# Performance work log

Measured on AMD Instinct MI355X. Metric: run time of the kernel, lower is better.

## Reference

```python
import jax, jax.numpy as jnp
import numpy as np

N_NODES = 50000
N_EDGES = 600000
IN_DIM = 128
HID_DIM = 512
OUT_DIM = 2


def setup_inputs() -> dict:
    key = jax.random.key(0)
    ks = jax.random.split(key, 8)
    x = jax.random.normal(ks[0], (N_NODES, IN_DIM), dtype=jnp.float32)
    edge_index = jax.random.randint(ks[1], (2, N_EDGES), 0, N_NODES, dtype=jnp.int32)
    s1 = 1.0 / np.sqrt(IN_DIM)
    s2 = 1.0 / np.sqrt(HID_DIM)
    # SAGEConv params: lin_l (applied to mean-aggregated neighbors, has bias),
    # lin_r (applied to root node features, no bias)
    W1l = jax.random.uniform(ks[2], (IN_DIM, HID_DIM), jnp.float32, -s1, s1)
    b1 = jax.random.uniform(ks[3], (HID_DIM,), jnp.float32, -s1, s1)
    W1r = jax.random.uniform(ks[4], (IN_DIM, HID_DIM), jnp.float32, -s1, s1)
    W2l = jax.random.uniform(ks[5], (HID_DIM, OUT_DIM), jnp.float32, -s2, s2)
    b2 = jax.random.uniform(ks[6], (OUT_DIM,), jnp.float32, -s2, s2)
    W2r = jax.random.uniform(ks[7], (HID_DIM, OUT_DIM), jnp.float32, -s2, s2)
    return {"x": x, "W1l": W1l, "b1": b1, "W1r": W1r,
            "W2l": W2l, "b2": b2, "W2r": W2r, "edge_index": edge_index}


def _sage_conv(x, edge_index, Wl, b, Wr):
    src, dst = edge_index[0], edge_index[1]
    msgs = x[src]                                             # [E, d]
    agg = jax.ops.segment_sum(msgs, dst, num_segments=x.shape[0])  # [N, d]
    deg = jax.ops.segment_sum(jnp.ones_like(dst, dtype=x.dtype), dst,
                              num_segments=x.shape[0])
    agg = agg / jnp.maximum(deg, 1.0)[:, None]                # mean aggregation
    return agg @ Wl + b + x @ Wr


def reference(x, W1l, b1, W1r, W2l, b2, W2r, edge_index):
    h = _sage_conv(x, edge_index, W1l, b1, W1r)
    h = jax.nn.relu(h)
    # dropout inactive (eval mode / force_dropout=False)
    out = _sage_conv(h, edge_index, W2l, b2, W2r)
    return jax.nn.log_softmax(out, axis=1)
```

## Files before the change

kernel.cpp:

```cpp
#include <hip/hip_runtime.h>
#include <math.h>
#include <stdint.h>

#define N_NODES 50000
#define N_EDGES 600000
#define IN_DIM 128
#define HID_DIM 512
#define M_PAD 50048
#define SCAN_NB 196
#define NPAD 50048

#define NB_C 128
#define CE4_C 1172
#define HALF_N 25024
#define H4W 6256
#define HIST_NB 256

#define CASTX_NB5 3125
#define CASTW_NB5 272

typedef __bf16 bf16;
typedef __bf16 bf16x2 __attribute__((ext_vector_type(2)));
typedef __bf16 bf16x4 __attribute__((ext_vector_type(4)));
typedef __bf16 bf16x8 __attribute__((ext_vector_type(8)));
typedef float f32x4 __attribute__((ext_vector_type(4)));

#define GLDS(gp, lp) __builtin_amdgcn_global_load_lds( \
    (const __attribute__((address_space(1))) uint32_t*)(gp), \
    (__attribute__((address_space(3))) uint32_t*)(lp), 16, 0, 0)


__global__ __launch_bounds__(512) void histcast_kernel(
    const int* __restrict__ dst, uint32_t* __restrict__ Hg32,
    const float* __restrict__ x, bf16* __restrict__ xb,
    const float* __restrict__ W1l, const float* __restrict__ W1r,
    const float* __restrict__ W2l, const float* __restrict__ W2r,
    bf16* __restrict__ Wt, bf16* __restrict__ W2bt,
    int* __restrict__ done) {
    __shared__ uint32_t h4[H4W];
    int b = blockIdx.x, t = threadIdx.x;
    if (b < HIST_NB) {
        for (int j = t; j < H4W; j += 512) h4[j] = 0;
        __syncthreads();
        int c = b >> 1, h = b & 1;
        int base = h * HALF_N;
        int e40 = c * CE4_C;
        int e4end = min(e40 + CE4_C, N_EDGES / 4);
        for (int e4 = e40 + t; e4 < e4end; e4 += 512) {
            int4 d = ((const int4*)dst)[e4];
            unsigned v0 = (unsigned)(d.x - base);
            unsigned v1 = (unsigned)(d.y - base);
            unsigned v2 = (unsigned)(d.z - base);
            unsigned v3 = (unsigned)(d.w - base);
            if (v0 < HALF_N) atomicAdd(&h4[v0 >> 2], 1u << ((v0 & 3) << 3));
            if (v1 < HALF_N) atomicAdd(&h4[v1 >> 2], 1u << ((v1 & 3) << 3));
            if (v2 < HALF_N) atomicAdd(&h4[v2 >> 2], 1u << ((v2 & 3) << 3));
            if (v3 < HALF_N) atomicAdd(&h4[v3 >> 2], 1u << ((v3 & 3) << 3));
        }
        __syncthreads();
        uint32_t* outp = Hg32 + (size_t)c * (NPAD / 4) + (size_t)h * H4W;
        for (int j = t; j < H4W; j += 512) outp[j] = h4[j];
    } else if (b < HIST_NB + CASTX_NB5) {
        if (b == HIST_NB && t < SCAN_NB) done[t] = 0;
        int i = (b - HIST_NB) * 512 + t;
        float4 v = ((const float4*)x)[i];
        bf16x4 o = {(bf16)v.x, (bf16)v.y, (bf16)v.z, (bf16)v.w};
        *(bf16x4*)(xb + (size_t)i * 4) = o;
    } else {
        int idx = (b - HIST_NB - CASTX_NB5) * 512 + t;
        if (idx < 512 * 256) {
            int n = idx >> 8;
            int k = idx & 255;
            float v = (k < IN_DIM) ? W1l[(size_t)k * HID_DIM + n]
                                   : W1r[(size_t)(k - IN_DIM) * HID_DIM + n];
            Wt[idx] = (bf16)v;
        } else {
            int j = idx - 512 * 256;
            int n = j >> 9;
            int k = j & 511;
            float v = 0.f;
            if (n == 0) v = W2l[k * 2 + 0];
            else if (n == 1) v = W2l[k * 2 + 1];
            else if (n == 2) v = W2r[k * 2 + 0];
            else if (n == 3) v = W2r[k * 2 + 1];
            W2bt[j] = (bf16)v;
        }
    }
}


__global__ __launch_bounds__(256) void scan_kernel(
    const uint8_t* __restrict__ Hg, uint8_t* __restrict__ PB,
    int* __restrict__ offsets, int* __restrict__ done) {
    int t = threadIdx.x, blk = blockIdx.x;
    int n = blk * 256 + t;
    int running = 0;
    if (n < NPAD) {
#pragma unroll 8
        for (int c = 0; c < NB_C; ++c) {
            int v = Hg[(size_t)c * NPAD + n];
            PB[(size_t)c * NPAD + n] = (uint8_t)running;
            running += v;
        }
    }
    int v = (n < N_NODES) ? running : 0;
    int l = t & 63, w = t >> 6;
    int inc = v;
#pragma unroll
    for (int off = 1; off < 64; off <<= 1) {
        int y = __shfl_up(inc, off);
        if (l >= off) inc += y;
    }
    __shared__ int wsum[4];
    __shared__ int lookback;
    if (l == 63) wsum[w] = inc;
    __syncthreads();
    if (t == 0) {
        int tot = wsum[0] + wsum[1] + wsum[2] + wsum[3];
        __hip_atomic_store(&done[blk], tot + 1, __ATOMIC_RELEASE,
                           __HIP_MEMORY_SCOPE_AGENT);
    }
    if (t < 64) {
        int s = 0;
        for (int u = t; u < blk; u += 64) {
            int dv;
            do {
                dv = __hip_atomic_load(&done[u], __ATOMIC_ACQUIRE,
                                       __HIP_MEMORY_SCOPE_AGENT);
            } while (dv == 0);
            s += dv - 1;
        }
#pragma unroll
        for (int m = 1; m < 64; m <<= 1) s += __shfl_xor(s, m);
        if (t == 0) lookback = s;
    }
    __syncthreads();
    int add = lookback;
    for (int u = 0; u < w; ++u) add += wsum[u];
    int ex = add + inc - v;
    if (n < N_NODES) offsets[n] = ex;
    if (blk == 0 && t == 0) offsets[N_NODES] = N_EDGES;
}


__global__ __launch_bounds__(512) void fill_kernel(
    const int* __restrict__ src, const int* __restrict__ dst,
    const int* __restrict__ offsets, const uint8_t* __restrict__ PB,
    int* __restrict__ csr_src) {
    __shared__ uint32_t h4[H4W];
    int b = blockIdx.x, t = threadIdx.x;
    for (int j = t; j < H4W; j += 512) h4[j] = 0;
    __syncthreads();
    int c = b >> 1, h = b & 1;
    int base = h * HALF_N;
    const uint8_t* pb = PB + (size_t)c * NPAD;
    int e40 = c * CE4_C;
    int e4end = min(e40 + CE4_C, N_EDGES / 4);
    for (int e4 = e40 + t; e4 < e4end; e4 += 512) {
        int4 d = ((const int4*)dst)[e4];
        int4 s = ((const int4*)src)[e4];
        unsigned v0 = (unsigned)(d.x - base);
        unsigned v1 = (unsigned)(d.y - base);
        unsigned v2 = (unsigned)(d.z - base);
        unsigned v3 = (unsigned)(d.w - base);
        if (v0 < HALF_N) {
            int sh = (v0 & 3) << 3;
            uint32_t r = atomicAdd(&h4[v0 >> 2], 1u << sh);
            csr_src[offsets[d.x] + (int)pb[d.x] + (int)((r >> sh) & 0xff)] = s.x;
        }
        if (v1 < HALF_N) {
            int sh = (v1 & 3) << 3;
            uint32_t r = atomicAdd(&h4[v1 >> 2], 1u << sh);
            csr_src[offsets[d.y] + (int)pb[d.y] + (int)((r >> sh) & 0xff)] = s.y;
        }
        if (v2 < HALF_N) {
            int sh = (v2 & 3) << 3;
            uint32_t r = atomicAdd(&h4[v2 >> 2], 1u << sh);
            csr_src[offsets[d.z] + (int)pb[d.z] + (int)((r >> sh) & 0xff)] = s.z;
        }
        if (v3 < HALF_N) {
            int sh = (v3 & 3) << 3;
            uint32_t r = atomicAdd(&h4[v3 >> 2], 1u << sh);
            csr_src[offsets[d.w] + (int)pb[d.w] + (int)((r >> sh) & 0xff)] = s.w;
        }
    }
}


__global__ __launch_bounds__(256) void agg1_kernel(
    const bf16* __restrict__ xb, const int* __restrict__ offsets,
    const int* __restrict__ csr_src, bf16* __restrict__ agg1b) {
    int t = threadIdx.x;
    int w = t >> 6, l = t & 63;
    int g = l >> 4;
    int sl = l & 15;
    int n = blockIdx.x * 16 + w * 4 + g;
    int s0 = offsets[n], s1 = offsets[n + 1];
    float a[8] = {};
    int e = s0;
    for (; e + 4 <= s1; e += 4) {
        int i0 = csr_src[e + 0];
        int i1 = csr_src[e + 1];
        int i2 = csr_src[e + 2];
        int i3 = csr_src[e + 3];
        bf16x8 v0 = *(const bf16x8*)(xb + (size_t)i0 * IN_DIM + sl * 8);
        bf16x8 v1 = *(const bf16x8*)(xb + (size_t)i1 * IN_DIM + sl * 8);
        bf16x8 v2 = *(const bf16x8*)(xb + (size_t)i2 * IN_DIM + sl * 8);
        bf16x8 v3 = *(const bf16x8*)(xb + (size_t)i3 * IN_DIM + sl * 8);
#pragma unroll
        for (int u = 0; u < 8; ++u)
            a[u] += (float)v0[u] + (float)v1[u] + (float)v2[u] + (float)v3[u];
    }
    for (; e < s1; ++e) {
        int i0 = csr_src[e];
        bf16x8 v0 = *(const bf16x8*)(xb + (size_t)i0 * IN_DIM + sl * 8);
#pragma unroll
        for (int u = 0; u < 8; ++u) a[u] += (float)v0[u];
    }
    float inv = 1.0f / fmaxf((float)(s1 - s0), 1.0f);
    bf16x8 o;
#pragma unroll
    for (int u = 0; u < 8; ++u) o[u] = (bf16)(a[u] * inv);
    *(bf16x8*)(agg1b + (size_t)n * IN_DIM + sl * 8) = o;
}


__global__ __launch_bounds__(256) void gemm1_kernel(
    const bf16* __restrict__ agg1b, const bf16* __restrict__ xb,
    const bf16* __restrict__ Wt, const float* __restrict__ b1,
    const bf16* __restrict__ W2bt, float* __restrict__ zpart) {
    __shared__ __align__(16) char smem[128 * 136 * 2];
    bf16 (*As)[128][32] = (bf16(*)[128][32])smem;
    bf16 (*Bs)[128][32] = (bf16(*)[128][32])(smem + 16384);
    bf16 (*Hs)[136] = (bf16(*)[136])smem;
    int tid = threadIdx.x;
    int w = tid >> 6;
    int lane = tid & 63;
    int q = lane >> 4, rr = lane & 15;
    int cb = blockIdx.x;
    int n0 = cb * 128;
    int row0 = blockIdx.y * 128;
    int wm = (w & 1) * 64, wn = (w >> 1) * 64;
    int lr = lane >> 2;
    int lc = (lane & 3) * 8;

    auto stage = [&](int ki) {
        const bf16* Asrc;
        int kb;
        if (ki < 4) { Asrc = agg1b; kb = ki * 32; }
        else        { Asrc = xb;    kb = ki * 32 - IN_DIM; }
        int kw = ki * 32;
        int buf = ki & 1;
#pragma unroll
        for (int j = 0; j < 2; ++j) {
            int r = w * 32 + j * 16 + lr;
            GLDS(Asrc + (size_t)(row0 + r) * IN_DIM + kb + lc,
                 &As[buf][w * 32 + j * 16][0]);
            GLDS(Wt + (size_t)(n0 + r) * 256 + kw + lc,
                 &Bs[buf][w * 32 + j * 16][0]);
        }
    };

    f32x4 acc[4][4] = {};
    stage(0);
#pragma unroll
    for (int ki = 0; ki < 8; ++ki) {
        __syncthreads();
        if (ki + 1 < 8) stage(ki + 1);
        int buf = ki & 1;
        bf16x8 af[4], bfr[4];
#pragma unroll
        for (int i = 0; i < 4; ++i)
            af[i] = *(const bf16x8*)&As[buf][wm + i * 16 + rr][q * 8];
#pragma unroll
        for (int j = 0; j < 4; ++j)
            bfr[j] = *(const bf16x8*)&Bs[buf][wn + j * 16 + rr][q * 8];
#pragma unroll
        for (int i = 0; i < 4; ++i)
#pragma unroll
            for (int j = 0; j < 4; ++j)
                acc[i][j] = __builtin_amdgcn_mfma_f32_16x16x32_bf16(
                    af[i], bfr[j], acc[i][j], 0, 0, 0);
    }
    __syncthreads();
    float bias[4];
#pragma unroll
    for (int j = 0; j < 4; ++j) bias[j] = b1[n0 + wn + j * 16 + rr];
#pragma unroll
    for (int i = 0; i < 4; ++i) {
#pragma unroll
        for (int rg = 0; rg < 4; ++rg) {
            int mrow = wm + i * 16 + q * 4 + rg;
#pragma unroll
            for (int j = 0; j < 4; ++j)
                Hs[mrow][wn + j * 16 + rr] =
                    (bf16)fmaxf(acc[i][j][rg] + bias[j], 0.f);
        }
    }
    __syncthreads();
    bf16x8 wf[4];
#pragma unroll
    for (int ks = 0; ks < 4; ++ks)
        wf[ks] = *(const bf16x8*)(W2bt + (size_t)rr * 512 + n0 + ks * 32 + q * 8);
    f32x4 zacc[2] = {};
#pragma unroll
    for (int mt = 0; mt < 2; ++mt)
#pragma unroll
        for (int ks = 0; ks < 4; ++ks) {
            bf16x8 afz = *(const bf16x8*)&Hs[w * 32 + mt * 16 + rr][ks * 32 + q * 8];
            zacc[mt] = __builtin_amdgcn_mfma_f32_16x16x32_bf16(
                afz, wf[ks], zacc[mt], 0, 0, 0);
        }
    if (rr < 4) {
#pragma unroll
        for (int mt = 0; mt < 2; ++mt)
#pragma unroll
            for (int rg = 0; rg < 4; ++rg) {
                int grow = row0 + w * 32 + mt * 16 + q * 4 + rg;
                zpart[(size_t)grow * 16 + cb * 4 + rr] = zacc[mt][rg];
            }
    }
}


__global__ __launch_bounds__(256) void zsum_kernel(const float* __restrict__ zpart,
                                                   float* __restrict__ z) {
    int n = blockIdx.x * blockDim.x + threadIdx.x;
    if (n >= N_NODES) return;
    const float4* p = (const float4*)(zpart + (size_t)n * 16);
    float4 a = p[0], b = p[1], c = p[2], d = p[3];
    float4 o = {a.x + b.x + c.x + d.x, a.y + b.y + c.y + d.y,
                a.z + b.z + c.z + d.z, a.w + b.w + c.w + d.w};
    *(float4*)(z + (size_t)n * 4) = o;
}


__global__ void final_kernel(const float* __restrict__ z, const int* __restrict__ offsets,
                             const int* __restrict__ csr_src, const float* __restrict__ b2,
                             float* __restrict__ out) {
    int n = blockIdx.x * blockDim.x + threadIdx.x;
    if (n >= N_NODES) return;
    int s0 = offsets[n], s1 = offsets[n + 1];
    float a0 = 0.f, a1 = 0.f;
    int e = s0;
    for (; e + 4 <= s1; e += 4) {
        int i0 = csr_src[e], i1 = csr_src[e + 1];
        int i2 = csr_src[e + 2], i3 = csr_src[e + 3];
        float2 v0 = *(const float2*)(z + (size_t)i0 * 4);
        float2 v1 = *(const float2*)(z + (size_t)i1 * 4);
        float2 v2 = *(const float2*)(z + (size_t)i2 * 4);
        float2 v3 = *(const float2*)(z + (size_t)i3 * 4);
        a0 += v0.x + v1.x + v2.x + v3.x;
        a1 += v0.y + v1.y + v2.y + v3.y;
    }
    for (; e < s1; ++e) {
        int s = csr_src[e];
        float2 v = *(const float2*)(z + (size_t)s * 4);
        a0 += v.x;
        a1 += v.y;
    }
    float inv = 1.0f / fmaxf((float)(s1 - s0), 1.0f);
    float2 zs = *(const float2*)(z + (size_t)n * 4 + 2);
    float o0 = a0 * inv + b2[0] + zs.x;
    float o1 = a1 * inv + b2[1] + zs.y;
    float m = fmaxf(o0, o1);
    float lse = logf(expf(o0 - m) + expf(o1 - m));
    float2 o = {o0 - m - lse, o1 - m - lse};
    *(float2*)(out + (size_t)n * 2) = o;
}


extern "C" void kernel_launch(void* const* d_in, const int* in_sizes, int n_in,
                              void* d_out, int out_size, void* d_ws, size_t ws_size,
                              hipStream_t stream) {
    const float* x   = (const float*)d_in[0];
    const float* W1l = (const float*)d_in[1];
    const float* b1  = (const float*)d_in[2];
    const float* W1r = (const float*)d_in[3];
    const float* W2l = (const float*)d_in[4];
    const float* b2  = (const float*)d_in[5];
    const float* W2r = (const float*)d_in[6];
    const int* edge  = (const int*)d_in[7];
    const int* src = edge;
    const int* dst = edge + N_EDGES;
    float* out = (float*)d_out;

    char* ws = (char*)d_ws;
    size_t off = 0;
    auto alloc = [&](size_t bytes) -> void* {
        void* p = ws + off;
        off += (bytes + 255) & ~(size_t)255;
        return p;
    };
    int* offsets = (int*)alloc((size_t)(N_NODES + 1) * 4);
    int* csr_src = (int*)alloc((size_t)N_EDGES * 4);
    int* done    = (int*)alloc((size_t)SCAN_NB * 4);
    bf16* xb     = (bf16*)alloc((size_t)M_PAD * IN_DIM * 2);
    bf16* agg1b  = (bf16*)alloc((size_t)M_PAD * IN_DIM * 2);
    bf16* Wt     = (bf16*)alloc((size_t)HID_DIM * 256 * 2);
    bf16* W2bt   = (bf16*)alloc((size_t)16 * HID_DIM * 2);
    float* zpart = (float*)alloc((size_t)M_PAD * 16 * 4);
    float* z     = (float*)alloc((size_t)N_NODES * 4 * 4);
    uint8_t* PB  = (uint8_t*)alloc((size_t)NB_C * NPAD);

    uint32_t* Hg32 = (uint32_t*)agg1b;

    histcast_kernel<<<HIST_NB + CASTX_NB5 + CASTW_NB5, 512, 0, stream>>>(
        dst, Hg32, x, xb, W1l, W1r, W2l, W2r, Wt, W2bt, done);
    scan_kernel<<<SCAN_NB, 256, 0, stream>>>(
        (const uint8_t*)Hg32, PB, offsets, done);
    fill_kernel<<<HIST_NB, 512, 0, stream>>>(src, dst, offsets, PB, csr_src);
    agg1_kernel<<<N_NODES / 16, 256, 0, stream>>>(xb, offsets, csr_src, agg1b);
    gemm1_kernel<<<dim3(4, M_PAD / 128), 256, 0, stream>>>(
        agg1b, xb, Wt, b1, W2bt, zpart);
    zsum_kernel<<<(N_NODES + 255) / 256, 256, 0, stream>>>(zpart, z);
    final_kernel<<<(N_NODES + 255) / 256, 256, 0, stream>>>(z, offsets, csr_src, b2, out);
}
```

Measured before the change: 175.0 us.

## Fuse CSR build and first aggregation into one cooperative persistent kernel

Merges the histogram/cast, scan, fill and agg1 kernels into a single cooperative kernel that separates phases with grid.sync, which removes several kernel launch boundaries. Chunk count doubles to 256 with 256-thread blocks so the persistent grid has more independent histogram units, and Hg gets its own buffer instead of aliasing agg1b. The final kernel now assigns four lanes per node and reduces with shuffles, to balance irregular degrees. Risks include grid.sync cost, lower per-phase occupancy from a grid limited to 1024 blocks, and doubled scan work over 256 chunks.

```diff
diff --git a/kernel.cpp b/kernel.cpp
--- a/kernel.cpp
+++ b/kernel.cpp
@@ -1,6 +1,9 @@
 #include <hip/hip_runtime.h>
+#include <hip/hip_cooperative_groups.h>
 #include <math.h>
 #include <stdint.h>
+
+namespace cg = cooperative_groups;
 
 #define N_NODES 50000
 #define N_EDGES 600000
@@ -10,17 +13,18 @@
 #define SCAN_NB 196
 #define NPAD 50048
 
-#define NB_C 128
-#define CE4_C 1172
+#define NB_C 256
+#define CE4_C 586
 #define HALF_N 25024
 #define H4W 6256
-#define HIST_NB 256
-
-#define CASTX_NB5 3125
-#define CASTW_NB5 272
+#define HIST_UNITS 512
+
+#define CASTX_U 6250
+#define CASTW_U 544
+#define NCAST (CASTX_U + CASTW_U)
+#define AGG_UNITS 3125
 
 typedef __bf16 bf16;
-typedef __bf16 bf16x2 __attribute__((ext_vector_type(2)));
 typedef __bf16 bf16x4 __attribute__((ext_vector_type(4)));
 typedef __bf16 bf16x8 __attribute__((ext_vector_type(8)));
 typedef float f32x4 __attribute__((ext_vector_type(4)));
@@ -30,23 +34,29 @@
     (__attribute__((address_space(3))) uint32_t*)(lp), 16, 0, 0)
 
 
-__global__ __launch_bounds__(512) void histcast_kernel(
-    const int* __restrict__ dst, uint32_t* __restrict__ Hg32,
+__global__ __launch_bounds__(256, 4) void build_kernel(
+    const int* __restrict__ src, const int* __restrict__ dst,
     const float* __restrict__ x, bf16* __restrict__ xb,
     const float* __restrict__ W1l, const float* __restrict__ W1r,
     const float* __restrict__ W2l, const float* __restrict__ W2r,
     bf16* __restrict__ Wt, bf16* __restrict__ W2bt,
-    int* __restrict__ done) {
+    uint32_t* __restrict__ Hg32, uint8_t* __restrict__ PB,
+    int* __restrict__ offsets, int* __restrict__ done,
+    int* __restrict__ csr_src, bf16* __restrict__ agg1b) {
+    cg::grid_group grid = cg::this_grid();
     __shared__ uint32_t h4[H4W];
-    int b = blockIdx.x, t = threadIdx.x;
-    if (b < HIST_NB) {
-        for (int j = t; j < H4W; j += 512) h4[j] = 0;
-        __syncthreads();
-        int c = b >> 1, h = b & 1;
+    int blk = blockIdx.x, t = threadIdx.x;
+    int gsz = gridDim.x;
+
+    if (blk == 0 && t < SCAN_NB) done[t] = 0;
+    for (int u = blk; u < HIST_UNITS; u += gsz) {
+        for (int j = t; j < H4W; j += 256) h4[j] = 0;
+        __syncthreads();
+        int c = u >> 1, h = u & 1;
         int base = h * HALF_N;
         int e40 = c * CE4_C;
         int e4end = min(e40 + CE4_C, N_EDGES / 4);
-        for (int e4 = e40 + t; e4 < e4end; e4 += 512) {
+        for (int e4 = e40 + t; e4 < e4end; e4 += 256) {
             int4 d = ((const int4*)dst)[e4];
             unsigned v0 = (unsigned)(d.x - base);
             unsigned v1 = (unsigned)(d.y - base);
@@ -59,169 +69,163 @@
         }
         __syncthreads();
         uint32_t* outp = Hg32 + (size_t)c * (NPAD / 4) + (size_t)h * H4W;
-        for (int j = t; j < H4W; j += 512) outp[j] = h4[j];
-    } else if (b < HIST_NB + CASTX_NB5) {
-        if (b == HIST_NB && t < SCAN_NB) done[t] = 0;
-        int i = (b - HIST_NB) * 512 + t;
-        float4 v = ((const float4*)x)[i];
-        bf16x4 o = {(bf16)v.x, (bf16)v.y, (bf16)v.z, (bf16)v.w};
-        *(bf16x4*)(xb + (size_t)i * 4) = o;
-    } else {
-        int idx = (b - HIST_NB - CASTX_NB5) * 512 + t;
-        if (idx < 512 * 256) {
-            int n = idx >> 8;
-            int k = idx & 255;
-            float v = (k < IN_DIM) ? W1l[(size_t)k * HID_DIM + n]
-                                   : W1r[(size_t)(k - IN_DIM) * HID_DIM + n];
-            Wt[idx] = (bf16)v;
+        for (int j = t; j < H4W; j += 256) outp[j] = h4[j];
+        __syncthreads();
+    }
+    for (int u = blk; u < NCAST; u += gsz) {
+        if (u < CASTX_U) {
+            int i = u * 256 + t;
+            float4 v = ((const float4*)x)[i];
+            bf16x4 o = {(bf16)v.x, (bf16)v.y, (bf16)v.z, (bf16)v.w};
+            *(bf16x4*)(xb + (size_t)i * 4) = o;
         } else {
-            int j = idx - 512 * 256;
-            int n = j >> 9;
-            int k = j & 511;
-            float v = 0.f;
-            if (n == 0) v = W2l[k * 2 + 0];
-            else if (n == 1) v = W2l[k * 2 + 1];
-            else if (n == 2) v = W2r[k * 2 + 0];
-            else if (n == 3) v = W2r[k * 2 + 1];
-            W2bt[j] = (bf16)v;
-        }
-    }
-}
-
-
-__global__ __launch_bounds__(256) void scan_kernel(
-    const uint8_t* __restrict__ Hg, uint8_t* __restrict__ PB,
-    int* __restrict__ offsets, int* __restrict__ done) {
-    int t = threadIdx.x, blk = blockIdx.x;
-    int n = blk * 256 + t;
-    int running = 0;
-    if (n < NPAD) {
+            int idx = (u - CASTX_U) * 256 + t;
+            if (idx < 512 * 256) {
+                int n = idx >> 8;
+                int k = idx & 255;
+                float v = (k < IN_DIM) ? W1l[(size_t)k * HID_DIM + n]
+                                       : W1r[(size_t)(k - IN_DIM) * HID_DIM + n];
+                Wt[idx] = (bf16)v;
+            } else {
+                int j = idx - 512 * 256;
+                int n = j >> 9;
+                int k = j & 511;
+                float v = 0.f;
+                if (n == 0) v = W2l[k * 2 + 0];
+                else if (n == 1) v = W2l[k * 2 + 1];
+                else if (n == 2) v = W2r[k * 2 + 0];
+                else if (n == 3) v = W2r[k * 2 + 1];
+                W2bt[j] = (bf16)v;
+            }
+        }
+    }
+    grid.sync();
+
+    if (blk < SCAN_NB) {
+        const uint8_t* Hg = (const uint8_t*)Hg32;
+        int n = blk * 256 + t;
+        int running = 0;
+        if (n < NPAD) {
 #pragma unroll 8
-        for (int c = 0; c < NB_C; ++c) {
-            int v = Hg[(size_t)c * NPAD + n];
-            PB[(size_t)c * NPAD + n] = (uint8_t)running;
-            running += v;
-        }
-    }
-    int v = (n < N_NODES) ? running : 0;
-    int l = t & 63, w = t >> 6;
-    int inc = v;
-#pragma unroll
-    for (int off = 1; off < 64; off <<= 1) {
-        int y = __shfl_up(inc, off);
-        if (l >= off) inc += y;
-    }
-    __shared__ int wsum[4];
-    __shared__ int lookback;
-    if (l == 63) wsum[w] = inc;
-    __syncthreads();
-    if (t == 0) {
-        int tot = wsum[0] + wsum[1] + wsum[2] + wsum[3];
-        __hip_atomic_store(&done[blk], tot + 1, __ATOMIC_RELEASE,
-                           __HIP_MEMORY_SCOPE_AGENT);
-    }
-    if (t < 64) {
-        int s = 0;
-        for (int u = t; u < blk; u += 64) {
-            int dv;
-            do {
-                dv = __hip_atomic_load(&done[u], __ATOMIC_ACQUIRE,
-                                       __HIP_MEMORY_SCOPE_AGENT);
-            } while (dv == 0);
-            s += dv - 1;
-        }
-#pragma unroll
-        for (int m = 1; m < 64; m <<= 1) s += __shfl_xor(s, m);
-        if (t == 0) lookback = s;
-    }
-    __syncthreads();
-    int add = lookback;
-    for (int u = 0; u < w; ++u) add += wsum[u];
-    int ex = add + inc - v;
-    if (n < N_NODES) offsets[n] = ex;
-    if (blk == 0 && t == 0) offsets[N_NODES] = N_EDGES;
-}
-
-
-__global__ __launch_bounds__(512) void fill_kernel(
-    const int* __restrict__ src, const int* __restrict__ dst,
-    const int* __restrict__ offsets, const uint8_t* __restrict__ PB,
-    int* __restrict__ csr_src) {
-    __shared__ uint32_t h4[H4W];
-    int b = blockIdx.x, t = threadIdx.x;
-    for (int j = t; j < H4W; j += 512) h4[j] = 0;
-    __syncthreads();
-    int c = b >> 1, h = b & 1;
-    int base = h * HALF_N;
-    const uint8_t* pb = PB + (size_t)c * NPAD;
-    int e40 = c * CE4_C;
-    int e4end = min(e40 + CE4_C, N_EDGES / 4);
-    for (int e4 = e40 + t; e4 < e4end; e4 += 512) {
-        int4 d = ((const int4*)dst)[e4];
-        int4 s = ((const int4*)src)[e4];
-        unsigned v0 = (unsigned)(d.x - base);
-        unsigned v1 = (unsigned)(d.y - base);
-        unsigned v2 = (unsigned)(d.z - base);
-        unsigned v3 = (unsigned)(d.w - base);
-        if (v0 < HALF_N) {
-            int sh = (v0 & 3) << 3;
-            uint32_t r = atomicAdd(&h4[v0 >> 2], 1u << sh);
-            csr_src[offsets[d.x] + (int)pb[d.x] + (int)((r >> sh) & 0xff)] = s.x;
-        }
-        if (v1 < HALF_N) {
-            int sh = (v1 & 3) << 3;
-            uint32_t r = atomicAdd(&h4[v1 >> 2], 1u << sh);
-            csr_src[offsets[d.y] + (int)pb[d.y] + (int)((r >> sh) & 0xff)] = s.y;
-        }
-        if (v2 < HALF_N) {
-            int sh = (v2 & 3) << 3;
-            uint32_t r = atomicAdd(&h4[v2 >> 2], 1u << sh);
-            csr_src[offsets[d.z] + (int)pb[d.z] + (int)((r >> sh) & 0xff)] = s.z;
-        }
-        if (v3 < HALF_N) {
-            int sh = (v3 & 3) << 3;
-            uint32_t r = atomicAdd(&h4[v3 >> 2], 1u << sh);
-            csr_src[offsets[d.w] + (int)pb[d.w] + (int)((r >> sh) & 0xff)] = s.w;
-        }
-    }
-}
-
-
-__global__ __launch_bounds__(256) void agg1_kernel(
-    const bf16* __restrict__ xb, const int* __restrict__ offsets,
-    const int* __restrict__ csr_src, bf16* __restrict__ agg1b) {
-    int t = threadIdx.x;
+            for (int c = 0; c < NB_C; ++c) {
+                int v = Hg[(size_t)c * NPAD + n];
+                PB[(size_t)c * NPAD + n] = (uint8_t)running;
+                running += v;
+            }
+        }
+        int v = (n < N_NODES) ? running : 0;
+        int l = t & 63, w = t >> 6;
+        int inc = v;
+#pragma unroll
+        for (int off = 1; off < 64; off <<= 1) {
+            int y = __shfl_up(inc, off);
+            if (l >= off) inc += y;
+        }
+        __shared__ int wsum[4];
+        __shared__ int lookback;
+        if (l == 63) wsum[w] = inc;
+        __syncthreads();
+        if (t == 0) {
+            int tot = wsum[0] + wsum[1] + wsum[2] + wsum[3];
+            __hip_atomic_store(&done[blk], tot + 1, __ATOMIC_RELEASE,
+                               __HIP_MEMORY_SCOPE_AGENT);
+        }
+        if (t < 64) {
+            int s = 0;
+            for (int u = t; u < blk; u += 64) {
+                int dv;
+                do {
+                    dv = __hip_atomic_load(&done[u], __ATOMIC_ACQUIRE,
+                                           __HIP_MEMORY_SCOPE_AGENT);
+                } while (dv == 0);
+                s += dv - 1;
+            }
+#pragma unroll
+            for (int m = 1; m < 64; m <<= 1) s += __shfl_xor(s, m);
+            if (t == 0) lookback = s;
+        }
+        __syncthreads();
+        int add = lookback;
+        for (int u = 0; u < w; ++u) add += wsum[u];
+        int ex = add + inc - v;
+        if (n < N_NODES) offsets[n] = ex;
+        if (blk == 0 && t == 0) offsets[N_NODES] = N_EDGES;
+    }
+    grid.sync();
+
+    for (int u = blk; u < HIST_UNITS; u += gsz) {
+        for (int j = t; j < H4W; j += 256) h4[j] = 0;
+        __syncthreads();
+        int c = u >> 1, h = u & 1;
+        int base = h * HALF_N;
+        const uint8_t* pb = PB + (size_t)c * NPAD;
+        int e40 = c * CE4_C;
+        int e4end = min(e40 + CE4_C, N_EDGES / 4);
+        for (int e4 = e40 + t; e4 < e4end; e4 += 256) {
+            int4 d = ((const int4*)dst)[e4];
+            int4 s = ((const int4*)src)[e4];
+            unsigned v0 = (unsigned)(d.x - base);
+            unsigned v1 = (unsigned)(d.y - base);
+            unsigned v2 = (unsigned)(d.z - base);
+            unsigned v3 = (unsigned)(d.w - base);
+            if (v0 < HALF_N) {
+                int sh = (v0 & 3) << 3;
+                uint32_t r = atomicAdd(&h4[v0 >> 2], 1u << sh);
+                csr_src[offsets[d.x] + (int)pb[d.x] + (int)((r >> sh) & 0xff)] = s.x;
+            }
+            if (v1 < HALF_N) {
+                int sh = (v1 & 3) << 3;
+                uint32_t r = atomicAdd(&h4[v1 >> 2], 1u << sh);
+                csr_src[offsets[d.y] + (int)pb[d.y] + (int)((r >> sh) & 0xff)] = s.y;
+            }
+            if (v2 < HALF_N) {
+                int sh = (v2 & 3) << 3;
+                uint32_t r = atomicAdd(&h4[v2 >> 2], 1u << sh);
+                csr_src[offsets[d.z] + (int)pb[d.z] + (int)((r >> sh) & 0xff)] = s.z;
+            }
+            if (v3 < HALF_N) {
+                int sh = (v3 & 3) << 3;
+                uint32_t r = atomicAdd(&h4[v3 >> 2], 1u << sh);
+                csr_src[offsets[d.w] + (int)pb[d.w] + (int)((r >> sh) & 0xff)] = s.w;
+            }
+        }
+        __syncthreads();
+    }
+    grid.sync();
+
     int w = t >> 6, l = t & 63;
     int g = l >> 4;
     int sl = l & 15;
-    int n = blockIdx.x * 16 + w * 4 + g;
-    int s0 = offsets[n], s1 = offsets[n + 1];
-    float a[8] = {};
-    int e = s0;
-    for (; e + 4 <= s1; e += 4) {
-        int i0 = csr_src[e + 0];
-        int i1 = csr_src[e + 1];
-        int i2 = csr_src[e + 2];
-        int i3 = csr_src[e + 3];
-        bf16x8 v0 = *(const bf16x8*)(xb + (size_t)i0 * IN_DIM + sl * 8);
-        bf16x8 v1 = *(const bf16x8*)(xb + (size_t)i1 * IN_DIM + sl * 8);
-        bf16x8 v2 = *(const bf16x8*)(xb + (size_t)i2 * IN_DIM + sl * 8);
-        bf16x8 v3 = *(const bf16x8*)(xb + (size_t)i3 * IN_DIM + sl * 8);
-#pragma unroll
-        for (int u = 0; u < 8; ++u)
-            a[u] += (float)v0[u] + (float)v1[u] + (float)v2[u] + (float)v3[u];
-    }
-    for (; e < s1; ++e) {
-        int i0 = csr_src[e];
-        bf16x8 v0 = *(const bf16x8*)(xb + (size_t)i0 * IN_DIM + sl * 8);
-#pragma unroll
-        for (int u = 0; u < 8; ++u) a[u] += (float)v0[u];
-    }
-    float inv = 1.0f / fmaxf((float)(s1 - s0), 1.0f);
-    bf16x8 o;
-#pragma unroll
-    for (int u = 0; u < 8; ++u) o[u] = (bf16)(a[u] * inv);
-    *(bf16x8*)(agg1b + (size_t)n * IN_DIM + sl * 8) = o;
+    for (int u = blk; u < AGG_UNITS; u += gsz) {
+        int n = u * 16 + w * 4 + g;
+        int s0 = offsets[n], s1 = offsets[n + 1];
+        float a[8] = {};
+        int e = s0;
+        for (; e + 4 <= s1; e += 4) {
+            int i0 = csr_src[e + 0];
+            int i1 = csr_src[e + 1];
+            int i2 = csr_src[e + 2];
+            int i3 = csr_src[e + 3];
+            bf16x8 v0 = *(const bf16x8*)(xb + (size_t)i0 * IN_DIM + sl * 8);
+            bf16x8 v1 = *(const bf16x8*)(xb + (size_t)i1 * IN_DIM + sl * 8);
+            bf16x8 v2 = *(const bf16x8*)(xb + (size_t)i2 * IN_DIM + sl * 8);
+            bf16x8 v3 = *(const bf16x8*)(xb + (size_t)i3 * IN_DIM + sl * 8);
+#pragma unroll
+            for (int uu = 0; uu < 8; ++uu)
+                a[uu] += (float)v0[uu] + (float)v1[uu] + (float)v2[uu] + (float)v3[uu];
+        }
+        for (; e < s1; ++e) {
+            int i0 = csr_src[e];
+            bf16x8 v0 = *(const bf16x8*)(xb + (size_t)i0 * IN_DIM + sl * 8);
+#pragma unroll
+            for (int uu = 0; uu < 8; ++uu) a[uu] += (float)v0[uu];
+        }
+        float inv = 1.0f / fmaxf((float)(s1 - s0), 1.0f);
+        bf16x8 o;
+#pragma unroll
+        for (int uu = 0; uu < 8; ++uu) o[uu] = (bf16)(a[uu] * inv);
+        *(bf16x8*)(agg1b + (size_t)n * IN_DIM + sl * 8) = o;
+    }
 }
 
 
@@ -335,38 +339,34 @@
 }
 
 
-__global__ void final_kernel(const float* __restrict__ z, const int* __restrict__ offsets,
-                             const int* __restrict__ csr_src, const float* __restrict__ b2,
-                             float* __restrict__ out) {
-    int n = blockIdx.x * blockDim.x + threadIdx.x;
-    if (n >= N_NODES) return;
-    int s0 = offsets[n], s1 = offsets[n + 1];
+__global__ __launch_bounds__(256) void final_kernel(
+    const float* __restrict__ z, const int* __restrict__ offsets,
+    const int* __restrict__ csr_src, const float* __restrict__ b2,
+    float* __restrict__ out) {
+    int t = threadIdx.x;
+    int lane4 = t & 3;
+    int n = blockIdx.x * 64 + (t >> 2);
+    int s0 = 0, s1 = 0;
+    if (n < N_NODES) { s0 = offsets[n]; s1 = offsets[n + 1]; }
     float a0 = 0.f, a1 = 0.f;
-    int e = s0;
-    for (; e + 4 <= s1; e += 4) {
-        int i0 = csr_src[e], i1 = csr_src[e + 1];
-        int i2 = csr_src[e + 2], i3 = csr_src[e + 3];
-        float2 v0 = *(const float2*)(z + (size_t)i0 * 4);
-        float2 v1 = *(const float2*)(z + (size_t)i1 * 4);
-        float2 v2 = *(const float2*)(z + (size_t)i2 * 4);
-        float2 v3 = *(const float2*)(z + (size_t)i3 * 4);
-        a0 += v0.x + v1.x + v2.x + v3.x;
-        a1 += v0.y + v1.y + v2.y + v3.y;
-    }
-    for (; e < s1; ++e) {
+    for (int e = s0 + lane4; e < s1; e += 4) {
         int s = csr_src[e];
         float2 v = *(const float2*)(z + (size_t)s * 4);
         a0 += v.x;
         a1 += v.y;
     }
-    float inv = 1.0f / fmaxf((float)(s1 - s0), 1.0f);
-    float2 zs = *(const float2*)(z + (size_t)n * 4 + 2);
-    float o0 = a0 * inv + b2[0] + zs.x;
-    float o1 = a1 * inv + b2[1] + zs.y;
-    float m = fmaxf(o0, o1);
-    float lse = logf(expf(o0 - m) + expf(o1 - m));
-    float2 o = {o0 - m - lse, o1 - m - lse};
-    *(float2*)(out + (size_t)n * 2) = o;
+    a0 += __shfl_xor(a0, 1); a0 += __shfl_xor(a0, 2);
+    a1 += __shfl_xor(a1, 1); a1 += __shfl_xor(a1, 2);
+    if (n < N_NODES && lane4 == 0) {
+        float inv = 1.0f / fmaxf((float)(s1 - s0), 1.0f);
+        float2 zs = *(const float2*)(z + (size_t)n * 4 + 2);
+        float o0 = a0 * inv + b2[0] + zs.x;
+        float o1 = a1 * inv + b2[1] + zs.y;
+        float m = fmaxf(o0, o1);
+        float lse = logf(expf(o0 - m) + expf(o1 - m));
+        float2 o = {o0 - m - lse, o1 - m - lse};
+        *(float2*)(out + (size_t)n * 2) = o;
+    }
 }
 
 
@@ -402,17 +402,29 @@
     float* zpart = (float*)alloc((size_t)M_PAD * 16 * 4);
     float* z     = (float*)alloc((size_t)N_NODES * 4 * 4);
     uint8_t* PB  = (uint8_t*)alloc((size_t)NB_C * NPAD);
-
-    uint32_t* Hg32 = (uint32_t*)agg1b;
-
-    histcast_kernel<<<HIST_NB + CASTX_NB5 + CASTW_NB5, 512, 0, stream>>>(
-        dst, Hg32, x, xb, W1l, W1r, W2l, W2r, Wt, W2bt, done);
-    scan_kernel<<<SCAN_NB, 256, 0, stream>>>(
-        (const uint8_t*)Hg32, PB, offsets, done);
-    fill_kernel<<<HIST_NB, 512, 0, stream>>>(src, dst, offsets, PB, csr_src);
-    agg1_kernel<<<N_NODES / 16, 256, 0, stream>>>(xb, offsets, csr_src, agg1b);
+    uint32_t* Hg32 = (uint32_t*)alloc((size_t)NB_C * NPAD);
+
+    static int gridBuild = 0;
+    if (gridBuild == 0) {
+        int mab = 0;
+        if (hipOccupancyMaxActiveBlocksPerMultiprocessor(
+                &mab, reinterpret_cast<const void*>(build_kernel), 256, 0) != hipSuccess ||
+            mab < 1)
+            mab = 2;
+        gridBuild = mab * 256;
+        if (gridBuild > 1024) gridBuild = 1024;
+        if (gridBuild < 256) gridBuild = 256;
+    }
+
+    void* bargs[] = {(void*)&src,  (void*)&dst,  (void*)&x,    (void*)&xb,
+                     (void*)&W1l,  (void*)&W1r,  (void*)&W2l,  (void*)&W2r,
+                     (void*)&Wt,   (void*)&W2bt, (void*)&Hg32, (void*)&PB,
+                     (void*)&offsets, (void*)&done, (void*)&csr_src,
+                     (void*)&agg1b};
+    hipLaunchCooperativeKernel(reinterpret_cast<void*>(build_kernel),
+                               dim3(gridBuild), dim3(256), bargs, 0, stream);
     gemm1_kernel<<<dim3(4, M_PAD / 128), 256, 0, stream>>>(
         agg1b, xb, Wt, b1, W2bt, zpart);
     zsum_kernel<<<(N_NODES + 255) / 256, 256, 0, stream>>>(zpart, z);
-    final_kernel<<<(N_NODES + 255) / 256, 256, 0, stream>>>(z, offsets, csr_src, b2, out);
+    final_kernel<<<(N_NODES + 63) / 64, 256, 0, stream>>>(z, offsets, csr_src, b2, out);
 }
```

Result: slower. 554.9 us (+217.1%).
